# Optimization experiments

Hardware: AMD Instinct MI355X
Metric: run time of the kernel (lower is better)

The kernel has to match this reference:

```python
import jax, jax.numpy as jnp
import numpy as np

N, S, H = 16, 2048, 1024
K = 8           # num_models (experts)
D = H // 4      # bottleneck = hidden_dim // ds_factor


def setup_inputs() -> dict:
    key = jax.random.key(0)
    k1, k2, k3, k4, k5, k6 = jax.random.split(key, 6)
    hidden_states = jax.random.normal(k1, (N, S, H), dtype=jnp.float32)
    p = jax.random.uniform(k2, (N, K), dtype=jnp.float32)
    prob = p / jnp.sum(p, axis=-1, keepdims=True)  # normalized routing probs
    std = 0.02
    w_down = jax.random.normal(k3, (K, D, H), dtype=jnp.float32) * std
    b_down = jax.random.normal(k4, (K, D), dtype=jnp.float32) * std
    w_up = jax.random.normal(k5, (K, H, D), dtype=jnp.float32) * std
    b_up = jax.random.normal(k6, (K, H), dtype=jnp.float32) * std
    return {"hidden_states": hidden_states, "prob": prob,
            "w_down": w_down, "b_down": b_down,
            "w_up": w_up, "b_up": b_up}


def merge_linear(x, prob, weight, bias):
    # weight: (K, out, in); prob: (N, K) -> per-instance merged weight (N, out, in)
    w = jnp.einsum('nk,koi->noi', prob, weight)
    b = jnp.einsum('nk,ko->no', prob, bias)
    # x: (N, S, in) -> (N, S, out); matmul with per-instance weight^T
    y = jnp.einsum('nsi,noi->nso', x, w)
    return y + b[:, None, :]


def reference(hidden_states, prob, w_down, b_down, w_up, b_up):
    # MergeAdapter forward (ln_before=False, ln_after=False, dropout=0)
    residual = merge_linear(hidden_states, prob, w_down, b_down)
    residual = jax.nn.relu(residual)
    residual = merge_linear(residual, prob, w_up, b_up)
    return hidden_states + residual
```

## Files before the change

kernel.cpp:

```cpp
#include <hip/hip_runtime.h>


typedef unsigned short u16;
typedef __bf16 bf16x8 __attribute__((ext_vector_type(8)));
typedef float f32x4 __attribute__((ext_vector_type(4)));

__device__ __forceinline__ u16 f2bf(float f) {
    union { float f; unsigned int i; } v; v.f = f;
    unsigned int r = v.i + 0x7fffu + ((v.i >> 16) & 1u);
    return (u16)(r >> 16);
}

__device__ __forceinline__ void gload_lds16(const u16* g, u16* l) {
    __builtin_amdgcn_global_load_lds(
        (const __attribute__((address_space(1))) void*)g,
        (__attribute__((address_space(3))) void*)l,
        16, 0, 0);
}

__device__ __forceinline__ void store8(u16* dst, float4 a, float4 b) {
    union { uint4 u; u16 s[8]; } cv;
    cv.s[0]=f2bf(a.x); cv.s[1]=f2bf(a.y); cv.s[2]=f2bf(a.z); cv.s[3]=f2bf(a.w);
    cv.s[4]=f2bf(b.x); cv.s[5]=f2bf(b.y); cv.s[6]=f2bf(b.z); cv.s[7]=f2bf(b.w);
    *(uint4*)dst = cv.u;
}

__global__ __launch_bounds__(256)
void merge_kernel(const float* __restrict__ prob,
                  const float* __restrict__ w_down, const float* __restrict__ b_down,
                  const float* __restrict__ w_up,   const float* __restrict__ b_up,
                  u16* __restrict__ Wd, u16* __restrict__ Wu,
                  float* __restrict__ bd, float* __restrict__ bu)
{
    __shared__ float sp[128];
    const int tid = threadIdx.x;
    if (tid < 128) sp[tid] = prob[tid];
    __syncthreads();

    const int bid = blockIdx.x;
    const int E = 256 * 1024;

    if (bid < 256) {
        int v = bid * 256 + tid;
        const bool down = (v < 32768);
        const int vv = down ? v : (v - 32768);
        const float* W = down ? w_down : w_up;
        u16* O = down ? Wd : Wu;
        const size_t e = (size_t)vv * 8;

        float wf[8][8];
        #pragma unroll
        for (int k = 0; k < 8; ++k) {
            const float4 f0 = *(const float4*)(W + (size_t)k * E + e);
            const float4 f1 = *(const float4*)(W + (size_t)k * E + e + 4);
            wf[k][0] = f0.x; wf[k][1] = f0.y; wf[k][2] = f0.z; wf[k][3] = f0.w;
            wf[k][4] = f1.x; wf[k][5] = f1.y; wf[k][6] = f1.z; wf[k][7] = f1.w;
        }
        for (int n = 0; n < 16; ++n) {
            float a[8] = {0.f,0.f,0.f,0.f,0.f,0.f,0.f,0.f};
            #pragma unroll
            for (int k = 0; k < 8; ++k) {
                const float p = sp[n * 8 + k];
                #pragma unroll
                for (int j = 0; j < 8; ++j) a[j] = fmaf(p, wf[k][j], a[j]);
            }
            union { uint4 u; u16 s[8]; } ov;
            #pragma unroll
            for (int j = 0; j < 8; ++j) ov.s[j] = f2bf(a[j]);
            *(uint4*)(O + (size_t)n * E + e) = ov.u;
        }
    } else {
        int idx = (bid - 256) * 256 + tid;
        if (idx < 16 * 256) {
            const int n = idx >> 8, d = idx & 255;
            float s = 0.f;
            #pragma unroll
            for (int k = 0; k < 8; ++k)
                s = fmaf(sp[n * 8 + k], b_down[k * 256 + d], s);
            bd[idx] = s;
        } else {
            const int i2 = idx - 4096;
            const int n = i2 >> 10, h = i2 & 1023;
            float s = 0.f;
            #pragma unroll
            for (int k = 0; k < 8; ++k)
                s = fmaf(sp[n * 8 + k], b_up[k * 1024 + h], s);
            bu[i2] = s;
        }
    }
}

__global__ __launch_bounds__(512, 4)
void fused_adapter(const float* __restrict__ x, const u16* __restrict__ Wd,
                   const u16* __restrict__ Wu, const float* __restrict__ bd,
                   const float* __restrict__ bu, float* __restrict__ out)
{
    __shared__ __align__(16) u16 lds[40960];

    const int tid  = threadIdx.x;
    const int lane = tid & 63;
    const int wave = tid >> 6;
    const int quad = lane >> 4, rl = lane & 15;
    const int rxl  = rl & 7;

    const int id = blockIdx.x;
    const int batch = (id & 7) * 2 + ((id >> 3) & 1);
    const int mblk  = id >> 4;

    const float* xb  = x  + (size_t)batch * 2048 * 1024 + (size_t)mblk * 64 * 1024;
    const u16*   Wdb = Wd + (size_t)batch * 256 * 1024;
    const u16*   Wub = Wu + (size_t)batch * 1024 * 256;
    const float* bdb = bd + batch * 256;
    const float* bub = bu + batch * 1024;
    float*       ob  = out + (size_t)batch * 2048 * 1024 + (size_t)mblk * 64 * 1024;

    const int wm1 = wave >> 2, wn1 = wave & 3;

    u16* const b0x = lds;          u16* const b0w = lds + 4096;
    u16* const b1x = lds + 20480;  u16* const b1w = lds + 24576;

    const int xrow = tid >> 3, xsl = tid & 7;
    const int xdst = (xrow * 8 + (xsl ^ (xrow & 7))) * 8;
    const int wrow  = tid >> 3;
    const int wgcol = ((tid & 7) ^ (wrow & 7)) * 8;

    f32x4 acc1[2][4] = {};

    {
        const float4 a0 = *(const float4*)(xb + (size_t)xrow * 1024 + xsl * 8);
        const float4 a1 = *(const float4*)(xb + (size_t)xrow * 1024 + xsl * 8 + 4);
        #pragma unroll
        for (int r = 0; r < 4; ++r)
            gload_lds16(Wdb + (size_t)(r * 64 + wrow) * 1024 + wgcol,
                        b0w + (size_t)(r * 512 + wave * 64) * 8);
        store8(b0x + xdst, a0, a1);
    }
    __syncthreads();

    for (int it = 0; it < 16; ++it) {
        u16* cx = (it & 1) ? b1x : b0x;
        u16* cw = (it & 1) ? b1w : b0w;
        u16* nx = (it & 1) ? b0x : b1x;
        u16* nw = (it & 1) ? b0w : b1w;
        const int k1 = (it + 1) * 64;

        float4 a0, a1;
        if (it < 15) {
            a0 = *(const float4*)(xb + (size_t)xrow * 1024 + k1 + xsl * 8);
            a1 = *(const float4*)(xb + (size_t)xrow * 1024 + k1 + xsl * 8 + 4);
            #pragma unroll
            for (int r = 0; r < 4; ++r)
                gload_lds16(Wdb + (size_t)(r * 64 + wrow) * 1024 + k1 + wgcol,
                            nw + (size_t)(r * 512 + wave * 64) * 8);
        }

        #pragma unroll
        for (int kk = 0; kk < 64; kk += 32) {
            bf16x8 av[2], bv[4];
            #pragma unroll
            for (int mi = 0; mi < 2; ++mi)
                av[mi] = *(const bf16x8*)(cx + (wm1 * 32 + mi * 16 + rl) * 64
                                          + ((kk / 8 + quad) ^ rxl) * 8);
            #pragma unroll
            for (int ni = 0; ni < 4; ++ni)
                bv[ni] = *(const bf16x8*)(cw + (wn1 * 64 + ni * 16 + rl) * 64
                                          + ((kk / 8 + quad) ^ rxl) * 8);
            #pragma unroll
            for (int mi = 0; mi < 2; ++mi)
                #pragma unroll
                for (int ni = 0; ni < 4; ++ni)
                    acc1[mi][ni] = __builtin_amdgcn_mfma_f32_16x16x32_bf16(
                        av[mi], bv[ni], acc1[mi][ni], 0, 0, 0);
        }

        if (it < 15) store8(nx + xdst, a0, a1);
        __syncthreads();
    }

    #pragma unroll
    for (int ni = 0; ni < 4; ++ni) {
        const int col = wn1 * 64 + ni * 16 + rl;
        const float bval = bdb[col];
        const int lbc = col >> 3, hi = lbc & 24, c7 = lbc & 7, cl = col & 7;
        #pragma unroll
        for (int mi = 0; mi < 2; ++mi)
            #pragma unroll
            for (int i = 0; i < 4; ++i) {
                const int row = wm1 * 32 + mi * 16 + quad * 4 + i;
                const int phys = hi | (c7 ^ (row & 7));
                lds[row * 256 + phys * 8 + cl] =
                    f2bf(fmaxf(acc1[mi][ni][i] + bval, 0.0f));
            }
    }
    __syncthreads();

    const int wm2 = wave >> 2, wn2 = wave & 3;

    const int srow = tid >> 5, ss = tid & 31;
    const int wugcol = ((ss & 24) | ((ss & 7) ^ (srow & 7))) * 8;

    auto stage_wu = [&](int c, u16* buf) {
        #pragma unroll
        for (int rr = 0; rr < 4; ++rr)
            gload_lds16(Wub + (size_t)(c * 64 + rr * 16 + srow) * 256 + wugcol,
                        buf + (size_t)(rr * 512 + wave * 64) * 8);
    };

    stage_wu(0, lds + 16384);

    bf16x8 af[2][8];
    #pragma unroll
    for (int mi = 0; mi < 2; ++mi) {
        const int rowb = (wm2 * 32 + mi * 16 + rl) * 256;
        #pragma unroll
        for (int t = 0; t < 8; ++t) {
            const int lb = t * 4 + quad;
            const int phys = (lb & 24) | ((lb & 7) ^ rxl);
            af[mi][t] = *(const bf16x8*)(lds + rowb + phys * 8);
        }
    }
    __syncthreads();

    u16* cur = lds + 16384;
    u16* nxt = lds;
    for (int c = 0; c < 16; ++c) {
        if (c < 15) stage_wu(c + 1, nxt);

        f32x4 acc2[2] = {};
        #pragma unroll
        for (int t = 0; t < 8; ++t) {
            const int lb = t * 4 + quad;
            const int phys = (lb & 24) | ((lb & 7) ^ rxl);
            const bf16x8 bv = *(const bf16x8*)(cur + (wn2 * 16 + rl) * 256
                                               + phys * 8);
            #pragma unroll
            for (int mi = 0; mi < 2; ++mi)
                acc2[mi] = __builtin_amdgcn_mfma_f32_16x16x32_bf16(
                    af[mi][t], bv, acc2[mi], 0, 0, 0);
        }

        const int colg = c * 64 + wn2 * 16 + rl;
        const float bval = bub[colg];
        #pragma unroll
        for (int mi = 0; mi < 2; ++mi)
            #pragma unroll
            for (int i = 0; i < 4; ++i) {
                const int rowl = wm2 * 32 + mi * 16 + quad * 4 + i;
                const size_t off = (size_t)rowl * 1024 + colg;
                ob[off] = acc2[mi][i] + bval + xb[off];
            }

        if (c < 15) {
            u16* t2 = cur; cur = nxt; nxt = t2;
            __syncthreads();
        }
    }
}

extern "C" void kernel_launch(void* const* d_in, const int* in_sizes, int n_in,
                              void* d_out, int out_size, void* d_ws, size_t ws_size,
                              hipStream_t stream) {
    const float* hidden = (const float*)d_in[0];
    const float* prob   = (const float*)d_in[1];
    const float* w_down = (const float*)d_in[2];
    const float* b_down = (const float*)d_in[3];
    const float* w_up   = (const float*)d_in[4];
    const float* b_up   = (const float*)d_in[5];
    float* out = (float*)d_out;

    u16* Wd = (u16*)d_ws;
    u16* Wu = Wd + (size_t)16 * 256 * 1024;
    float* bd = (float*)(Wu + (size_t)16 * 1024 * 256);
    float* bu = bd + 16 * 256;

    merge_kernel<<<336, 256, 0, stream>>>(prob, w_down, b_down, w_up, b_up,
                                          Wd, Wu, bd, bu);

    fused_adapter<<<512, 512, 0, stream>>>(hidden, Wd, Wu, bd, bu, out);
}
```

Before: 320.4 us.

## Double M tile to 128 rows with triple-buffered K pipeline and manual waitcnts

Each block now processes 128 rows instead of 64, halving the grid and doubling per-block reuse of the merged down/up weights. The down-projection loop uses a three-stage LDS ring with explicit vmcnt/lgkmcnt waits and raw s_barrier in place of __syncthreads. The up-projection prefetches the residual x and bias into registers one chunk ahead. The aim is to cut weight reloads and barrier stalls, at the cost of more LDS (144KB), lower occupancy and fragile hand-counted wait values.

```diff
diff --git a/kernel.cpp b/kernel.cpp
--- a/kernel.cpp
+++ b/kernel.cpp
@@ -23,6 +23,14 @@
     cv.s[0]=f2bf(a.x); cv.s[1]=f2bf(a.y); cv.s[2]=f2bf(a.z); cv.s[3]=f2bf(a.w);
     cv.s[4]=f2bf(b.x); cv.s[5]=f2bf(b.y); cv.s[6]=f2bf(b.z); cv.s[7]=f2bf(b.w);
     *(uint4*)dst = cv.u;
+}
+
+#define MEMF() asm volatile("" ::: "memory")
+
+__device__ __forceinline__ void barx() {
+    asm volatile("" ::: "memory");
+    __builtin_amdgcn_s_barrier();
+    asm volatile("" ::: "memory");
 }
 
 __global__ __launch_bounds__(256)
@@ -90,12 +98,12 @@
     }
 }
 
-__global__ __launch_bounds__(512, 4)
+__global__ __launch_bounds__(512, 2)
 void fused_adapter(const float* __restrict__ x, const u16* __restrict__ Wd,
                    const u16* __restrict__ Wu, const float* __restrict__ bd,
                    const float* __restrict__ bu, float* __restrict__ out)
 {
-    __shared__ __align__(16) u16 lds[40960];
+    __shared__ __align__(16) u16 lds[73728];
 
     const int tid  = threadIdx.x;
     const int lane = tid & 63;
@@ -107,152 +115,205 @@
     const int batch = (id & 7) * 2 + ((id >> 3) & 1);
     const int mblk  = id >> 4;
 
-    const float* xb  = x  + (size_t)batch * 2048 * 1024 + (size_t)mblk * 64 * 1024;
+    const float* xb  = x  + (size_t)batch * 2048 * 1024 + (size_t)mblk * 128 * 1024;
     const u16*   Wdb = Wd + (size_t)batch * 256 * 1024;
     const u16*   Wub = Wu + (size_t)batch * 1024 * 256;
     const float* bdb = bd + batch * 256;
     const float* bub = bu + batch * 1024;
-    float*       ob  = out + (size_t)batch * 2048 * 1024 + (size_t)mblk * 64 * 1024;
+    float*       ob  = out + (size_t)batch * 2048 * 1024 + (size_t)mblk * 128 * 1024;
+
+    constexpr int XO[3] = {0, 24576, 49152};
+    constexpr int WO[3] = {8192, 32768, 57344};
 
     const int wm1 = wave >> 2, wn1 = wave & 3;
 
-    u16* const b0x = lds;          u16* const b0w = lds + 4096;
-    u16* const b1x = lds + 20480;  u16* const b1w = lds + 24576;
-
-    const int xrow = tid >> 3, xsl = tid & 7;
-    const int xdst = (xrow * 8 + (xsl ^ (xrow & 7))) * 8;
+    const int xrow = tid >> 2;
+    const int xcs  = (tid & 3) * 16;
+    const int s0   = (tid & 3) * 2;
+    const int xd0  = (xrow * 8 + (s0 ^ (xrow & 7))) * 8;
+    const int xd1  = (xrow * 8 + ((s0 + 1) ^ (xrow & 7))) * 8;
     const int wrow  = tid >> 3;
     const int wgcol = ((tid & 7) ^ (wrow & 7)) * 8;
 
-    f32x4 acc1[2][4] = {};
-
-    {
-        const float4 a0 = *(const float4*)(xb + (size_t)xrow * 1024 + xsl * 8);
-        const float4 a1 = *(const float4*)(xb + (size_t)xrow * 1024 + xsl * 8 + 4);
+    float bdv[4];
+    #pragma unroll
+    for (int ni = 0; ni < 4; ++ni) bdv[ni] = bdb[wn1 * 64 + ni * 16 + rl];
+    MEMF();
+
+    auto ldx = [&](int kt, float4* d) {
+        const float* p = xb + (size_t)xrow * 1024 + kt + xcs;
+        d[0] = *(const float4*)(p);
+        d[1] = *(const float4*)(p + 4);
+        d[2] = *(const float4*)(p + 8);
+        d[3] = *(const float4*)(p + 12);
+    };
+    auto stx = [&](u16* xbuf, const float4* d) {
+        store8(xbuf + xd0, d[0], d[1]);
+        store8(xbuf + xd1, d[2], d[3]);
+    };
+    auto stage_wd = [&](int kt, u16* wbuf) {
         #pragma unroll
         for (int r = 0; r < 4; ++r)
-            gload_lds16(Wdb + (size_t)(r * 64 + wrow) * 1024 + wgcol,
-                        b0w + (size_t)(r * 512 + wave * 64) * 8);
-        store8(b0x + xdst, a0, a1);
-    }
-    __syncthreads();
-
-    for (int it = 0; it < 16; ++it) {
-        u16* cx = (it & 1) ? b1x : b0x;
-        u16* cw = (it & 1) ? b1w : b0w;
-        u16* nx = (it & 1) ? b0x : b1x;
-        u16* nw = (it & 1) ? b0w : b1w;
-        const int k1 = (it + 1) * 64;
-
-        float4 a0, a1;
-        if (it < 15) {
-            a0 = *(const float4*)(xb + (size_t)xrow * 1024 + k1 + xsl * 8);
-            a1 = *(const float4*)(xb + (size_t)xrow * 1024 + k1 + xsl * 8 + 4);
-            #pragma unroll
-            for (int r = 0; r < 4; ++r)
-                gload_lds16(Wdb + (size_t)(r * 64 + wrow) * 1024 + k1 + wgcol,
-                            nw + (size_t)(r * 512 + wave * 64) * 8);
-        }
-
-        #pragma unroll
-        for (int kk = 0; kk < 64; kk += 32) {
-            bf16x8 av[2], bv[4];
-            #pragma unroll
-            for (int mi = 0; mi < 2; ++mi)
-                av[mi] = *(const bf16x8*)(cx + (wm1 * 32 + mi * 16 + rl) * 64
-                                          + ((kk / 8 + quad) ^ rxl) * 8);
-            #pragma unroll
-            for (int ni = 0; ni < 4; ++ni)
-                bv[ni] = *(const bf16x8*)(cw + (wn1 * 64 + ni * 16 + rl) * 64
-                                          + ((kk / 8 + quad) ^ rxl) * 8);
-            #pragma unroll
-            for (int mi = 0; mi < 2; ++mi)
+            gload_lds16(Wdb + (size_t)(r * 64 + wrow) * 1024 + kt + wgcol,
+                        wbuf + r * 4096 + wave * 512);
+    };
+
+    f32x4 acc1[4][4] = {};
+    auto comp1 = [&](const u16* xbuf, const u16* wbuf) {
+        #pragma unroll
+        for (int kk = 0; kk < 2; ++kk) {
+            bf16x8 av[4], bv[4];
+            #pragma unroll
+            for (int mi = 0; mi < 4; ++mi) {
+                const int row = wm1 * 64 + mi * 16 + rl;
+                av[mi] = *(const bf16x8*)(xbuf + (row * 8 + ((kk * 4 + quad) ^ rxl)) * 8);
+            }
+            #pragma unroll
+            for (int ni = 0; ni < 4; ++ni) {
+                const int row = wn1 * 64 + ni * 16 + rl;
+                bv[ni] = *(const bf16x8*)(wbuf + (row * 8 + ((kk * 4 + quad) ^ rxl)) * 8);
+            }
+            #pragma unroll
+            for (int mi = 0; mi < 4; ++mi)
                 #pragma unroll
                 for (int ni = 0; ni < 4; ++ni)
                     acc1[mi][ni] = __builtin_amdgcn_mfma_f32_16x16x32_bf16(
                         av[mi], bv[ni], acc1[mi][ni], 0, 0, 0);
         }
-
-        if (it < 15) store8(nx + xdst, a0, a1);
-        __syncthreads();
-    }
+    };
+
+    float4 xa[2][4];
+    ldx(0, xa[0]);  stage_wd(0, lds + WO[0]);
+    MEMF();
+    ldx(64, xa[1]); stage_wd(64, lds + WO[1]);
+    asm volatile("s_waitcnt vmcnt(12)" ::: "memory");
+    stx(lds + XO[0], xa[0]);
+    asm volatile("s_waitcnt vmcnt(8)" ::: "memory");
+    asm volatile("s_waitcnt lgkmcnt(0)" ::: "memory");
+    barx();
+
+    #pragma unroll
+    for (int t = 0; t < 16; ++t) {
+        const int cb = t % 3, nb1 = (t + 1) % 3, nb2 = (t + 2) % 3;
+        if (t < 14) {
+            ldx((t + 2) * 64, xa[t & 1]);
+            stage_wd((t + 2) * 64, lds + WO[nb2]);
+        }
+        comp1(lds + XO[cb], lds + WO[cb]);
+        if (t < 14)       asm volatile("s_waitcnt vmcnt(8)" ::: "memory");
+        else if (t == 14) asm volatile("s_waitcnt vmcnt(0)" ::: "memory");
+        if (t < 15) {
+            stx(lds + XO[nb1], xa[(t + 1) & 1]);
+            asm volatile("s_waitcnt lgkmcnt(0)" ::: "memory");
+        }
+        barx();
+    }
+
+    const int wm2 = wave >> 1, wn2 = wave & 1;
+    const int srow = tid >> 5, ss = tid & 31;
+    const int wugcol = ((ss & 24) | ((ss & 7) ^ (srow & 7))) * 8;
+    u16* const wub0 = lds + 32768;
+    u16* const wub1 = lds + 49152;
+
+    auto stage_wu = [&](int c, u16* buf) {
+        #pragma unroll
+        for (int rr = 0; rr < 4; ++rr)
+            gload_lds16(Wub + (size_t)(c * 64 + rr * 16 + srow) * 256 + wugcol,
+                        buf + rr * 4096 + wave * 512);
+    };
+    auto ldxqb = [&](int c, float* dq) {
+        #pragma unroll
+        for (int ni = 0; ni < 2; ++ni) {
+            const int colg = c * 64 + wn2 * 32 + ni * 16 + rl;
+            #pragma unroll
+            for (int mi = 0; mi < 2; ++mi)
+                #pragma unroll
+                for (int i = 0; i < 4; ++i)
+                    dq[ni * 8 + mi * 4 + i] =
+                        xb[(size_t)(wm2 * 32 + mi * 16 + quad * 4 + i) * 1024 + colg];
+            dq[16 + ni] = bub[colg];
+        }
+    };
+
+    stage_wu(0, wub0);
+    MEMF();
+    float xqb[2][18];
+    ldxqb(0, xqb[0]);
 
     #pragma unroll
     for (int ni = 0; ni < 4; ++ni) {
         const int col = wn1 * 64 + ni * 16 + rl;
-        const float bval = bdb[col];
         const int lbc = col >> 3, hi = lbc & 24, c7 = lbc & 7, cl = col & 7;
         #pragma unroll
-        for (int mi = 0; mi < 2; ++mi)
+        for (int mi = 0; mi < 4; ++mi)
             #pragma unroll
             for (int i = 0; i < 4; ++i) {
-                const int row = wm1 * 32 + mi * 16 + quad * 4 + i;
+                const int row = wm1 * 64 + mi * 16 + quad * 4 + i;
                 const int phys = hi | (c7 ^ (row & 7));
                 lds[row * 256 + phys * 8 + cl] =
-                    f2bf(fmaxf(acc1[mi][ni][i] + bval, 0.0f));
-            }
-    }
-    __syncthreads();
-
-    const int wm2 = wave >> 2, wn2 = wave & 3;
-
-    const int srow = tid >> 5, ss = tid & 31;
-    const int wugcol = ((ss & 24) | ((ss & 7) ^ (srow & 7))) * 8;
-
-    auto stage_wu = [&](int c, u16* buf) {
-        #pragma unroll
-        for (int rr = 0; rr < 4; ++rr)
-            gload_lds16(Wub + (size_t)(c * 64 + rr * 16 + srow) * 256 + wugcol,
-                        buf + (size_t)(rr * 512 + wave * 64) * 8);
-    };
-
-    stage_wu(0, lds + 16384);
+                    f2bf(fmaxf(acc1[mi][ni][i] + bdv[ni], 0.0f));
+            }
+    }
+    asm volatile("s_waitcnt lgkmcnt(0)" ::: "memory");
+    asm volatile("s_waitcnt vmcnt(18)" ::: "memory");
+    barx();
 
     bf16x8 af[2][8];
     #pragma unroll
     for (int mi = 0; mi < 2; ++mi) {
-        const int rowb = (wm2 * 32 + mi * 16 + rl) * 256;
+        const int row = wm2 * 32 + mi * 16 + rl;
         #pragma unroll
         for (int t = 0; t < 8; ++t) {
             const int lb = t * 4 + quad;
             const int phys = (lb & 24) | ((lb & 7) ^ rxl);
-            af[mi][t] = *(const bf16x8*)(lds + rowb + phys * 8);
-        }
-    }
-    __syncthreads();
-
-    u16* cur = lds + 16384;
-    u16* nxt = lds;
+            af[mi][t] = *(const bf16x8*)(lds + (row * 32 + phys) * 8);
+        }
+    }
+
+    #pragma unroll
     for (int c = 0; c < 16; ++c) {
-        if (c < 15) stage_wu(c + 1, nxt);
-
-        f32x4 acc2[2] = {};
+        const u16* wcur = (c & 1) ? wub1 : wub0;
+        if (c < 15) {
+            ldxqb(c + 1, xqb[(c + 1) & 1]);
+            MEMF();
+            stage_wu(c + 1, (c & 1) ? wub0 : wub1);
+        }
+        f32x4 acc2[2][2] = {};
         #pragma unroll
         for (int t = 0; t < 8; ++t) {
-            const int lb = t * 4 + quad;
-            const int phys = (lb & 24) | ((lb & 7) ^ rxl);
-            const bf16x8 bv = *(const bf16x8*)(cur + (wn2 * 16 + rl) * 256
-                                               + phys * 8);
+            bf16x8 bv[2];
+            #pragma unroll
+            for (int ni = 0; ni < 2; ++ni) {
+                const int row = wn2 * 32 + ni * 16 + rl;
+                const int lb = t * 4 + quad;
+                const int phys = (lb & 24) | ((lb & 7) ^ rxl);
+                bv[ni] = *(const bf16x8*)(wcur + (row * 32 + phys) * 8);
+            }
             #pragma unroll
             for (int mi = 0; mi < 2; ++mi)
-                acc2[mi] = __builtin_amdgcn_mfma_f32_16x16x32_bf16(
-                    af[mi][t], bv, acc2[mi], 0, 0, 0);
-        }
-
-        const int colg = c * 64 + wn2 * 16 + rl;
-        const float bval = bub[colg];
-        #pragma unroll
-        for (int mi = 0; mi < 2; ++mi)
-            #pragma unroll
-            for (int i = 0; i < 4; ++i) {
-                const int rowl = wm2 * 32 + mi * 16 + quad * 4 + i;
-                const size_t off = (size_t)rowl * 1024 + colg;
-                ob[off] = acc2[mi][i] + bval + xb[off];
-            }
-
+                #pragma unroll
+                for (int ni = 0; ni < 2; ++ni)
+                    acc2[mi][ni] = __builtin_amdgcn_mfma_f32_16x16x32_bf16(
+                        af[mi][t], bv[ni], acc2[mi][ni], 0, 0, 0);
+        }
+        if (c < 15) asm volatile("s_waitcnt vmcnt(22)" ::: "memory");
+
+        #pragma unroll
+        for (int ni = 0; ni < 2; ++ni) {
+            const int colg = c * 64 + wn2 * 32 + ni * 16 + rl;
+            const float bval = xqb[c & 1][16 + ni];
+            #pragma unroll
+            for (int mi = 0; mi < 2; ++mi)
+                #pragma unroll
+                for (int i = 0; i < 4; ++i) {
+                    const int rowl = wm2 * 32 + mi * 16 + quad * 4 + i;
+                    ob[(size_t)rowl * 1024 + colg] =
+                        acc2[mi][ni][i] + bval + xqb[c & 1][ni * 8 + mi * 4 + i];
+                }
+        }
         if (c < 15) {
-            u16* t2 = cur; cur = nxt; nxt = t2;
-            __syncthreads();
+            asm volatile("s_waitcnt vmcnt(16)" ::: "memory");
+            barx();
         }
     }
 }
@@ -276,5 +337,5 @@
     merge_kernel<<<336, 256, 0, stream>>>(prob, w_down, b_down, w_up, b_up,
                                           Wd, Wu, bd, bu);
 
-    fused_adapter<<<512, 512, 0, stream>>>(hidden, Wd, Wu, bd, bu, out);
-}
+    fused_adapter<<<256, 512, 0, stream>>>(hidden, Wd, Wu, bd, bu, out);
+}
```

Result: faster. 300.3 us (-6.3%).

## Triple-buffer down-proj K loop with manual waitcnt and prefetch residual loads

Applied to the files above, without the earlier changes.

Restructures the first GEMM loop to use K-steps of 32 with a three-stage LDS ring buffer and prefetch distance two. Full __syncthreads are replaced with raw s_barrier plus hand-placed vmcnt/lgkmcnt waits, and s_setprio is raised around the MFMA blocks. In the up-projection loop the residual x and bias values are prefetched one chunk ahead into registers, and the down bias is hoisted. LDS usage shrinks, which may allow more blocks per CU, but the hand-counted wait counts are fragile and a miscount would cause races.

```diff
diff --git a/kernel.cpp b/kernel.cpp
--- a/kernel.cpp
+++ b/kernel.cpp
@@ -18,11 +18,18 @@
         16, 0, 0);
 }
 
-__device__ __forceinline__ void store8(u16* dst, float4 a, float4 b) {
-    union { uint4 u; u16 s[8]; } cv;
+__device__ __forceinline__ void store4(u16* dst, float4 a) {
+    union { uint2 u; u16 s[4]; } cv;
     cv.s[0]=f2bf(a.x); cv.s[1]=f2bf(a.y); cv.s[2]=f2bf(a.z); cv.s[3]=f2bf(a.w);
-    cv.s[4]=f2bf(b.x); cv.s[5]=f2bf(b.y); cv.s[6]=f2bf(b.z); cv.s[7]=f2bf(b.w);
-    *(uint4*)dst = cv.u;
+    *(uint2*)dst = cv.u;
+}
+
+#define MEMF() asm volatile("" ::: "memory")
+
+__device__ __forceinline__ void barx() {
+    asm volatile("" ::: "memory");
+    __builtin_amdgcn_s_barrier();
+    asm volatile("" ::: "memory");
 }
 
 __global__ __launch_bounds__(256)
@@ -95,7 +102,7 @@
                    const u16* __restrict__ Wu, const float* __restrict__ bd,
                    const float* __restrict__ bu, float* __restrict__ out)
 {
-    __shared__ __align__(16) u16 lds[40960];
+    __shared__ __align__(16) u16 lds[32768];
 
     const int tid  = threadIdx.x;
     const int lane = tid & 63;
@@ -114,73 +121,117 @@
     const float* bub = bu + batch * 1024;
     float*       ob  = out + (size_t)batch * 2048 * 1024 + (size_t)mblk * 64 * 1024;
 
+    constexpr int XO[3] = {0, 10240, 20480};
+    constexpr int WO[3] = {2048, 12288, 22528};
+
     const int wm1 = wave >> 2, wn1 = wave & 3;
 
-    u16* const b0x = lds;          u16* const b0w = lds + 4096;
-    u16* const b1x = lds + 20480;  u16* const b1w = lds + 24576;
-
-    const int xrow = tid >> 3, xsl = tid & 7;
-    const int xdst = (xrow * 8 + (xsl ^ (xrow & 7))) * 8;
-    const int wrow  = tid >> 3;
-    const int wgcol = ((tid & 7) ^ (wrow & 7)) * 8;
+    const int xrow = tid >> 3;
+    const int xc4  = (tid & 7) * 4;
+    const int xs2  = (tid & 7) >> 1, xhalf = tid & 1;
+    const int xdst = xrow * 32 + (xs2 ^ (xrow & 3)) * 8 + xhalf * 4;
+    const int wswz = ((lane & 3) ^ ((lane >> 2) & 3)) * 8;
+
+    float bdv[4];
+    #pragma unroll
+    for (int ni = 0; ni < 4; ++ni) bdv[ni] = bdb[wn1 * 64 + ni * 16 + rl];
+    asm volatile("s_waitcnt vmcnt(0)" ::: "memory");
+
+    auto ldx = [&](int kt, float4& d) {
+        d = *(const float4*)(xb + (size_t)xrow * 1024 + kt + xc4);
+    };
+    auto stx = [&](u16* xbuf, const float4& d) { store4(xbuf + xdst, d); };
+    auto stage_wd = [&](int kt, u16* wbuf) {
+        #pragma unroll
+        for (int r = 0; r < 2; ++r)
+            gload_lds16(Wdb + (size_t)((wave * 2 + r) * 16 + (lane >> 2)) * 1024
+                            + kt + wswz,
+                        wbuf + (wave * 2 + r) * 512);
+    };
 
     f32x4 acc1[2][4] = {};
-
-    {
-        const float4 a0 = *(const float4*)(xb + (size_t)xrow * 1024 + xsl * 8);
-        const float4 a1 = *(const float4*)(xb + (size_t)xrow * 1024 + xsl * 8 + 4);
-        #pragma unroll
-        for (int r = 0; r < 4; ++r)
-            gload_lds16(Wdb + (size_t)(r * 64 + wrow) * 1024 + wgcol,
-                        b0w + (size_t)(r * 512 + wave * 64) * 8);
-        store8(b0x + xdst, a0, a1);
-    }
-    __syncthreads();
-
-    for (int it = 0; it < 16; ++it) {
-        u16* cx = (it & 1) ? b1x : b0x;
-        u16* cw = (it & 1) ? b1w : b0w;
-        u16* nx = (it & 1) ? b0x : b1x;
-        u16* nw = (it & 1) ? b0w : b1w;
-        const int k1 = (it + 1) * 64;
-
-        float4 a0, a1;
-        if (it < 15) {
-            a0 = *(const float4*)(xb + (size_t)xrow * 1024 + k1 + xsl * 8);
-            a1 = *(const float4*)(xb + (size_t)xrow * 1024 + k1 + xsl * 8 + 4);
-            #pragma unroll
-            for (int r = 0; r < 4; ++r)
-                gload_lds16(Wdb + (size_t)(r * 64 + wrow) * 1024 + k1 + wgcol,
-                            nw + (size_t)(r * 512 + wave * 64) * 8);
-        }
-
-        #pragma unroll
-        for (int kk = 0; kk < 64; kk += 32) {
-            bf16x8 av[2], bv[4];
-            #pragma unroll
-            for (int mi = 0; mi < 2; ++mi)
-                av[mi] = *(const bf16x8*)(cx + (wm1 * 32 + mi * 16 + rl) * 64
-                                          + ((kk / 8 + quad) ^ rxl) * 8);
+    auto comp1 = [&](const u16* xbuf, const u16* wbuf) {
+        bf16x8 av[2], bv[4];
+        #pragma unroll
+        for (int mi = 0; mi < 2; ++mi) {
+            const int row = wm1 * 32 + mi * 16 + rl;
+            av[mi] = *(const bf16x8*)(xbuf + row * 32 + (quad ^ (row & 3)) * 8);
+        }
+        #pragma unroll
+        for (int ni = 0; ni < 4; ++ni) {
+            const int row = wn1 * 64 + ni * 16 + rl;
+            bv[ni] = *(const bf16x8*)(wbuf + row * 32 + (quad ^ (row & 3)) * 8);
+        }
+        __builtin_amdgcn_s_setprio(1);
+        #pragma unroll
+        for (int mi = 0; mi < 2; ++mi)
             #pragma unroll
             for (int ni = 0; ni < 4; ++ni)
-                bv[ni] = *(const bf16x8*)(cw + (wn1 * 64 + ni * 16 + rl) * 64
-                                          + ((kk / 8 + quad) ^ rxl) * 8);
-            #pragma unroll
-            for (int mi = 0; mi < 2; ++mi)
-                #pragma unroll
-                for (int ni = 0; ni < 4; ++ni)
-                    acc1[mi][ni] = __builtin_amdgcn_mfma_f32_16x16x32_bf16(
-                        av[mi], bv[ni], acc1[mi][ni], 0, 0, 0);
-        }
-
-        if (it < 15) store8(nx + xdst, a0, a1);
-        __syncthreads();
-    }
+                acc1[mi][ni] = __builtin_amdgcn_mfma_f32_16x16x32_bf16(
+                    av[mi], bv[ni], acc1[mi][ni], 0, 0, 0);
+        __builtin_amdgcn_s_setprio(0);
+    };
+
+    float4 xa[2];
+    ldx(0, xa[0]);  stage_wd(0, lds + WO[0]);
+    MEMF();
+    ldx(32, xa[1]); stage_wd(32, lds + WO[1]);
+    asm volatile("s_waitcnt vmcnt(5)" ::: "memory");
+    stx(lds + XO[0], xa[0]);
+    asm volatile("s_waitcnt vmcnt(3)" ::: "memory");
+    asm volatile("s_waitcnt lgkmcnt(0)" ::: "memory");
+    barx();
+
+    #pragma unroll
+    for (int t = 0; t < 32; ++t) {
+        const int cb = t % 3;
+        if (t < 30) {
+            ldx((t + 2) * 32, xa[t & 1]);
+            stage_wd((t + 2) * 32, lds + WO[(t + 2) % 3]);
+            MEMF();
+        }
+        comp1(lds + XO[cb], lds + WO[cb]);
+        if (t < 30)       asm volatile("s_waitcnt vmcnt(3)" ::: "memory");
+        else if (t == 30) asm volatile("s_waitcnt vmcnt(0)" ::: "memory");
+        if (t < 31) {
+            stx(lds + XO[(t + 1) % 3], xa[(t + 1) & 1]);
+            asm volatile("s_waitcnt lgkmcnt(0)" ::: "memory");
+        }
+        barx();
+    }
+
+    const int wm2 = wave >> 2, wn2 = wave & 3;
+    const int srow = tid >> 5, ss = tid & 31;
+    const int wugcol = ((ss & 24) | ((ss & 7) ^ (srow & 7))) * 8;
+    u16* const wub0 = lds + 16384;
+    u16* const wub1 = lds;
+
+    auto stage_wu = [&](int c, u16* buf) {
+        #pragma unroll
+        for (int rr = 0; rr < 4; ++rr)
+            gload_lds16(Wub + (size_t)(c * 64 + rr * 16 + srow) * 256 + wugcol,
+                        buf + (size_t)(rr * 512 + wave * 64) * 8);
+    };
+    auto ldxqb = [&](int c, float* dq) {
+        const int colg = c * 64 + wn2 * 16 + rl;
+        #pragma unroll
+        for (int mi = 0; mi < 2; ++mi)
+            #pragma unroll
+            for (int i = 0; i < 4; ++i)
+                dq[mi * 4 + i] =
+                    xb[(size_t)(wm2 * 32 + mi * 16 + quad * 4 + i) * 1024 + colg];
+        dq[8] = bub[colg];
+    };
+
+    stage_wu(0, wub0);
+    MEMF();
+    float xq[2][9];
+    ldxqb(0, xq[0]);
+    MEMF();
 
     #pragma unroll
     for (int ni = 0; ni < 4; ++ni) {
         const int col = wn1 * 64 + ni * 16 + rl;
-        const float bval = bdb[col];
         const int lbc = col >> 3, hi = lbc & 24, c7 = lbc & 7, cl = col & 7;
         #pragma unroll
         for (int mi = 0; mi < 2; ++mi)
@@ -189,70 +240,67 @@
                 const int row = wm1 * 32 + mi * 16 + quad * 4 + i;
                 const int phys = hi | (c7 ^ (row & 7));
                 lds[row * 256 + phys * 8 + cl] =
-                    f2bf(fmaxf(acc1[mi][ni][i] + bval, 0.0f));
+                    f2bf(fmaxf(acc1[mi][ni][i] + bdv[ni], 0.0f));
             }
     }
-    __syncthreads();
-
-    const int wm2 = wave >> 2, wn2 = wave & 3;
-
-    const int srow = tid >> 5, ss = tid & 31;
-    const int wugcol = ((ss & 24) | ((ss & 7) ^ (srow & 7))) * 8;
-
-    auto stage_wu = [&](int c, u16* buf) {
-        #pragma unroll
-        for (int rr = 0; rr < 4; ++rr)
-            gload_lds16(Wub + (size_t)(c * 64 + rr * 16 + srow) * 256 + wugcol,
-                        buf + (size_t)(rr * 512 + wave * 64) * 8);
-    };
-
-    stage_wu(0, lds + 16384);
+    asm volatile("s_waitcnt lgkmcnt(0)" ::: "memory");
+    asm volatile("s_waitcnt vmcnt(9)" ::: "memory");
+    barx();
 
     bf16x8 af[2][8];
     #pragma unroll
     for (int mi = 0; mi < 2; ++mi) {
-        const int rowb = (wm2 * 32 + mi * 16 + rl) * 256;
+        const int row = wm2 * 32 + mi * 16 + rl;
         #pragma unroll
         for (int t = 0; t < 8; ++t) {
             const int lb = t * 4 + quad;
             const int phys = (lb & 24) | ((lb & 7) ^ rxl);
-            af[mi][t] = *(const bf16x8*)(lds + rowb + phys * 8);
-        }
-    }
-    __syncthreads();
-
-    u16* cur = lds + 16384;
-    u16* nxt = lds;
+            af[mi][t] = *(const bf16x8*)(lds + (row * 32 + phys) * 8);
+        }
+    }
+    asm volatile("s_waitcnt lgkmcnt(0)" ::: "memory");
+    barx();
+
+    #pragma unroll
     for (int c = 0; c < 16; ++c) {
-        if (c < 15) stage_wu(c + 1, nxt);
-
+        const u16* wcur = (c & 1) ? wub1 : wub0;
+        if (c < 15) {
+            ldxqb(c + 1, xq[(c + 1) & 1]);
+            MEMF();
+            stage_wu(c + 1, (c & 1) ? wub0 : wub1);
+            MEMF();
+        }
         f32x4 acc2[2] = {};
+        __builtin_amdgcn_s_setprio(1);
         #pragma unroll
         for (int t = 0; t < 8; ++t) {
             const int lb = t * 4 + quad;
             const int phys = (lb & 24) | ((lb & 7) ^ rxl);
-            const bf16x8 bv = *(const bf16x8*)(cur + (wn2 * 16 + rl) * 256
+            const bf16x8 bv = *(const bf16x8*)(wcur + (wn2 * 16 + rl) * 256
                                                + phys * 8);
             #pragma unroll
             for (int mi = 0; mi < 2; ++mi)
                 acc2[mi] = __builtin_amdgcn_mfma_f32_16x16x32_bf16(
                     af[mi][t], bv, acc2[mi], 0, 0, 0);
         }
-
-        const int colg = c * 64 + wn2 * 16 + rl;
-        const float bval = bub[colg];
-        #pragma unroll
-        for (int mi = 0; mi < 2; ++mi)
-            #pragma unroll
-            for (int i = 0; i < 4; ++i) {
-                const int rowl = wm2 * 32 + mi * 16 + quad * 4 + i;
-                const size_t off = (size_t)rowl * 1024 + colg;
-                ob[off] = acc2[mi][i] + bval + xb[off];
-            }
-
+        __builtin_amdgcn_s_setprio(0);
+        if (c == 0) asm volatile("s_waitcnt vmcnt(13)" ::: "memory");
+
+        {
+            const int colg = c * 64 + wn2 * 16 + rl;
+            const float bval = xq[c & 1][8];
+            #pragma unroll
+            for (int mi = 0; mi < 2; ++mi)
+                #pragma unroll
+                for (int i = 0; i < 4; ++i) {
+                    const int rowl = wm2 * 32 + mi * 16 + quad * 4 + i;
+                    ob[(size_t)rowl * 1024 + colg] =
+                        acc2[mi][i] + bval + xq[c & 1][mi * 4 + i];
+                }
+        }
         if (c < 15) {
-            u16* t2 = cur; cur = nxt; nxt = t2;
-            __syncthreads();
+            asm volatile("s_waitcnt vmcnt(8)" ::: "memory");
+            barx();
         }
     }
 }
```

Measured after the change: 463.2 us. 44.6% more time.

## Split fused adapter into separate down and up projection kernels with bf16 intermediate

Applied to the files above, without the earlier changes.

Replaces the single fused down+up kernel with a down kernel that writes the ReLU bottleneck activations to a bf16 workspace, and an up kernel over many more blocks that tiles the output columns. The down kernel now loads x straight from global into registers and converts it to bf16 there, instead of staging it through LDS. The aim is more parallelism and occupancy in the up projection, which had a long serial loop per block. The cost is an extra pass reading x for the residual, plus the intermediate write and read.

```diff
diff --git a/kernel.cpp b/kernel.cpp
--- a/kernel.cpp
+++ b/kernel.cpp
@@ -9,6 +9,13 @@
     union { float f; unsigned int i; } v; v.f = f;
     unsigned int r = v.i + 0x7fffu + ((v.i >> 16) & 1u);
     return (u16)(r >> 16);
+}
+
+__device__ __forceinline__ bf16x8 cvt8(float4 a, float4 b) {
+    union { bf16x8 v; u16 s[8]; } r;
+    r.s[0]=f2bf(a.x); r.s[1]=f2bf(a.y); r.s[2]=f2bf(a.z); r.s[3]=f2bf(a.w);
+    r.s[4]=f2bf(b.x); r.s[5]=f2bf(b.y); r.s[6]=f2bf(b.z); r.s[7]=f2bf(b.w);
+    return r.v;
 }
 
 __device__ __forceinline__ void gload_lds16(const u16* g, u16* l) {
@@ -16,13 +23,6 @@
         (const __attribute__((address_space(1))) void*)g,
         (__attribute__((address_space(3))) void*)l,
         16, 0, 0);
-}
-
-__device__ __forceinline__ void store8(u16* dst, float4 a, float4 b) {
-    union { uint4 u; u16 s[8]; } cv;
-    cv.s[0]=f2bf(a.x); cv.s[1]=f2bf(a.y); cv.s[2]=f2bf(a.z); cv.s[3]=f2bf(a.w);
-    cv.s[4]=f2bf(b.x); cv.s[5]=f2bf(b.y); cv.s[6]=f2bf(b.z); cv.s[7]=f2bf(b.w);
-    *(uint4*)dst = cv.u;
 }
 
 __global__ __launch_bounds__(256)
@@ -90,18 +90,16 @@
     }
 }
 
-__global__ __launch_bounds__(512, 4)
-void fused_adapter(const float* __restrict__ x, const u16* __restrict__ Wd,
-                   const u16* __restrict__ Wu, const float* __restrict__ bd,
-                   const float* __restrict__ bu, float* __restrict__ out)
+__global__ __launch_bounds__(256, 2)
+void down_kernel(const float* __restrict__ x, const u16* __restrict__ Wd,
+                 const float* __restrict__ bd, u16* __restrict__ R)
 {
-    __shared__ __align__(16) u16 lds[40960];
+    __shared__ __align__(16) u16 wdl[2][8192];
 
     const int tid  = threadIdx.x;
     const int lane = tid & 63;
     const int wave = tid >> 6;
     const int quad = lane >> 4, rl = lane & 15;
-    const int rxl  = rl & 7;
 
     const int id = blockIdx.x;
     const int batch = (id & 7) * 2 + ((id >> 3) & 1);
@@ -109,151 +107,158 @@
 
     const float* xb  = x  + (size_t)batch * 2048 * 1024 + (size_t)mblk * 64 * 1024;
     const u16*   Wdb = Wd + (size_t)batch * 256 * 1024;
-    const u16*   Wub = Wu + (size_t)batch * 1024 * 256;
     const float* bdb = bd + batch * 256;
-    const float* bub = bu + batch * 1024;
-    float*       ob  = out + (size_t)batch * 2048 * 1024 + (size_t)mblk * 64 * 1024;
-
-    const int wm1 = wave >> 2, wn1 = wave & 3;
-
-    u16* const b0x = lds;          u16* const b0w = lds + 4096;
-    u16* const b1x = lds + 20480;  u16* const b1w = lds + 24576;
-
-    const int xrow = tid >> 3, xsl = tid & 7;
-    const int xdst = (xrow * 8 + (xsl ^ (xrow & 7))) * 8;
-    const int wrow  = tid >> 3;
-    const int wgcol = ((tid & 7) ^ (wrow & 7)) * 8;
-
-    f32x4 acc1[2][4] = {};
-
-    {
-        const float4 a0 = *(const float4*)(xb + (size_t)xrow * 1024 + xsl * 8);
-        const float4 a1 = *(const float4*)(xb + (size_t)xrow * 1024 + xsl * 8 + 4);
-        #pragma unroll
-        for (int r = 0; r < 4; ++r)
-            gload_lds16(Wdb + (size_t)(r * 64 + wrow) * 1024 + wgcol,
-                        b0w + (size_t)(r * 512 + wave * 64) * 8);
-        store8(b0x + xdst, a0, a1);
-    }
+    u16*         Rb  = R  + (size_t)batch * 2048 * 256 + (size_t)mblk * 64 * 256;
+
+    float bdv[4];
+    #pragma unroll
+    for (int ni = 0; ni < 4; ++ni) bdv[ni] = bdb[wave * 64 + ni * 16 + rl];
+
+    const int srow = lane >> 2, sslot = lane & 3;
+    auto stage = [&](int it, int b) {
+        const int kt = it * 32;
+        #pragma unroll
+        for (int r = 0; r < 4; ++r) {
+            const int row = r * 64 + wave * 16 + srow;
+            gload_lds16(Wdb + (size_t)row * 1024 + kt + ((sslot ^ (row & 3)) * 8),
+                        wdl[b] + r * 2048 + wave * 512);
+        }
+    };
+
+    auto ldA = [&](int it, bf16x8* av) {
+        #pragma unroll
+        for (int mi = 0; mi < 4; ++mi) {
+            const float* p = xb + (size_t)(mi * 16 + rl) * 1024 + it * 32 + quad * 8;
+            av[mi] = cvt8(*(const float4*)p, *(const float4*)(p + 4));
+        }
+    };
+
+    f32x4 acc[4][4] = {};
+    auto comp = [&](const u16* buf, const bf16x8* av) {
+        #pragma unroll
+        for (int ni = 0; ni < 4; ++ni) {
+            const int c = wave * 64 + ni * 16 + rl;
+            const bf16x8 bv = *(const bf16x8*)(buf + c * 32 + (quad ^ (rl & 3)) * 8);
+            #pragma unroll
+            for (int mi = 0; mi < 4; ++mi)
+                acc[mi][ni] = __builtin_amdgcn_mfma_f32_16x16x32_bf16(
+                    av[mi], bv, acc[mi][ni], 0, 0, 0);
+        }
+    };
+
+    bf16x8 avA[4], avB[4];
+    ldA(0, avA);
+    stage(0, 0);
     __syncthreads();
 
-    for (int it = 0; it < 16; ++it) {
-        u16* cx = (it & 1) ? b1x : b0x;
-        u16* cw = (it & 1) ? b1w : b0w;
-        u16* nx = (it & 1) ? b0x : b1x;
-        u16* nw = (it & 1) ? b0w : b1w;
-        const int k1 = (it + 1) * 64;
-
-        float4 a0, a1;
-        if (it < 15) {
-            a0 = *(const float4*)(xb + (size_t)xrow * 1024 + k1 + xsl * 8);
-            a1 = *(const float4*)(xb + (size_t)xrow * 1024 + k1 + xsl * 8 + 4);
-            #pragma unroll
-            for (int r = 0; r < 4; ++r)
-                gload_lds16(Wdb + (size_t)(r * 64 + wrow) * 1024 + k1 + wgcol,
-                            nw + (size_t)(r * 512 + wave * 64) * 8);
-        }
-
-        #pragma unroll
-        for (int kk = 0; kk < 64; kk += 32) {
-            bf16x8 av[2], bv[4];
-            #pragma unroll
-            for (int mi = 0; mi < 2; ++mi)
-                av[mi] = *(const bf16x8*)(cx + (wm1 * 32 + mi * 16 + rl) * 64
-                                          + ((kk / 8 + quad) ^ rxl) * 8);
-            #pragma unroll
-            for (int ni = 0; ni < 4; ++ni)
-                bv[ni] = *(const bf16x8*)(cw + (wn1 * 64 + ni * 16 + rl) * 64
-                                          + ((kk / 8 + quad) ^ rxl) * 8);
-            #pragma unroll
-            for (int mi = 0; mi < 2; ++mi)
+    #pragma unroll 2
+    for (int p = 0; p < 16; ++p) {
+        const int e = 2 * p;
+        if (e < 31) { stage(e + 1, 1); ldA(e + 1, avB); }
+        comp(wdl[0], avA);
+        __syncthreads();
+        const int o = e + 1;
+        if (o < 31) { stage(o + 1, 0); ldA(o + 1, avA); }
+        comp(wdl[1], avB);
+        __syncthreads();
+    }
+
+    #pragma unroll
+    for (int ni = 0; ni < 4; ++ni) {
+        const int col = wave * 64 + ni * 16 + rl;
+        #pragma unroll
+        for (int mi = 0; mi < 4; ++mi)
+            #pragma unroll
+            for (int i = 0; i < 4; ++i) {
+                const int row = mi * 16 + quad * 4 + i;
+                Rb[(size_t)row * 256 + col] =
+                    f2bf(fmaxf(acc[mi][ni][i] + bdv[ni], 0.0f));
+            }
+    }
+}
+
+__global__ __launch_bounds__(256, 4)
+void up_kernel(const float* __restrict__ x, const u16* __restrict__ Wu,
+               const float* __restrict__ bu, const u16* __restrict__ R,
+               float* __restrict__ out)
+{
+    __shared__ __align__(16) u16 wul[2][8192];
+
+    const int tid  = threadIdx.x;
+    const int lane = tid & 63;
+    const int wave = tid >> 6;
+    const int quad = lane >> 4, rl = lane & 15;
+
+    const int id = blockIdx.x;
+    const int batch = (id & 7) * 2 + ((id >> 3) & 1);
+    const int rest  = id >> 4;
+    const int mblk  = rest & 31;
+    const int nblk  = rest >> 5;
+
+    const u16* Rb = R + (size_t)batch * 2048 * 256 + (size_t)mblk * 64 * 256;
+    const size_t base = (size_t)batch * 2048 * 1024 + (size_t)mblk * 64 * 1024
+                      + (size_t)nblk * 128;
+    const float* xb  = x + base;
+    float*       ob  = out + base;
+    const u16*   Wub = Wu + (size_t)batch * 1024 * 256 + (size_t)nblk * 128 * 256;
+    const float* bub2 = bu + batch * 1024 + nblk * 128;
+
+    float buv[2];
+    #pragma unroll
+    for (int ni = 0; ni < 2; ++ni) buv[ni] = bub2[wave * 32 + ni * 16 + rl];
+
+    const int srow = lane >> 3, sslot = lane & 7;
+    auto stage = [&](int it, int b) {
+        const int kt = it * 64;
+        #pragma unroll
+        for (int r = 0; r < 4; ++r) {
+            const int row = r * 32 + wave * 8 + srow;
+            gload_lds16(Wub + (size_t)row * 256 + kt + ((sslot ^ (row & 7)) * 8),
+                        wul[b] + r * 2048 + wave * 512);
+        }
+    };
+
+    f32x4 acc[4][2] = {};
+
+    stage(0, 0);
+    __syncthreads();
+
+    #pragma unroll
+    for (int it = 0; it < 4; ++it) {
+        const int cur = it & 1;
+        if (it < 3) stage(it + 1, cur ^ 1);
+        #pragma unroll
+        for (int kk = 0; kk < 2; ++kk) {
+            bf16x8 av[4];
+            #pragma unroll
+            for (int mi = 0; mi < 4; ++mi)
+                av[mi] = *(const bf16x8*)(Rb + (size_t)(mi * 16 + rl) * 256
+                                          + it * 64 + kk * 32 + quad * 8);
+            #pragma unroll
+            for (int ni = 0; ni < 2; ++ni) {
+                const int c = wave * 32 + ni * 16 + rl;
+                const bf16x8 bv = *(const bf16x8*)(wul[cur] + c * 64
+                                    + (((kk * 4 + quad) ^ (rl & 7)) * 8));
                 #pragma unroll
-                for (int ni = 0; ni < 4; ++ni)
-                    acc1[mi][ni] = __builtin_amdgcn_mfma_f32_16x16x32_bf16(
-                        av[mi], bv[ni], acc1[mi][ni], 0, 0, 0);
-        }
-
-        if (it < 15) store8(nx + xdst, a0, a1);
+                for (int mi = 0; mi < 4; ++mi)
+                    acc[mi][ni] = __builtin_amdgcn_mfma_f32_16x16x32_bf16(
+                        av[mi], bv, acc[mi][ni], 0, 0, 0);
+            }
+        }
         __syncthreads();
     }
 
     #pragma unroll
-    for (int ni = 0; ni < 4; ++ni) {
-        const int col = wn1 * 64 + ni * 16 + rl;
-        const float bval = bdb[col];
-        const int lbc = col >> 3, hi = lbc & 24, c7 = lbc & 7, cl = col & 7;
-        #pragma unroll
-        for (int mi = 0; mi < 2; ++mi)
+    for (int ni = 0; ni < 2; ++ni) {
+        const int coll = wave * 32 + ni * 16 + rl;
+        #pragma unroll
+        for (int mi = 0; mi < 4; ++mi)
             #pragma unroll
             for (int i = 0; i < 4; ++i) {
-                const int row = wm1 * 32 + mi * 16 + quad * 4 + i;
-                const int phys = hi | (c7 ^ (row & 7));
-                lds[row * 256 + phys * 8 + cl] =
-                    f2bf(fmaxf(acc1[mi][ni][i] + bval, 0.0f));
-            }
-    }
-    __syncthreads();
-
-    const int wm2 = wave >> 2, wn2 = wave & 3;
-
-    const int srow = tid >> 5, ss = tid & 31;
-    const int wugcol = ((ss & 24) | ((ss & 7) ^ (srow & 7))) * 8;
-
-    auto stage_wu = [&](int c, u16* buf) {
-        #pragma unroll
-        for (int rr = 0; rr < 4; ++rr)
-            gload_lds16(Wub + (size_t)(c * 64 + rr * 16 + srow) * 256 + wugcol,
-                        buf + (size_t)(rr * 512 + wave * 64) * 8);
-    };
-
-    stage_wu(0, lds + 16384);
-
-    bf16x8 af[2][8];
-    #pragma unroll
-    for (int mi = 0; mi < 2; ++mi) {
-        const int rowb = (wm2 * 32 + mi * 16 + rl) * 256;
-        #pragma unroll
-        for (int t = 0; t < 8; ++t) {
-            const int lb = t * 4 + quad;
-            const int phys = (lb & 24) | ((lb & 7) ^ rxl);
-            af[mi][t] = *(const bf16x8*)(lds + rowb + phys * 8);
-        }
-    }
-    __syncthreads();
-
-    u16* cur = lds + 16384;
-    u16* nxt = lds;
-    for (int c = 0; c < 16; ++c) {
-        if (c < 15) stage_wu(c + 1, nxt);
-
-        f32x4 acc2[2] = {};
-        #pragma unroll
-        for (int t = 0; t < 8; ++t) {
-            const int lb = t * 4 + quad;
-            const int phys = (lb & 24) | ((lb & 7) ^ rxl);
-            const bf16x8 bv = *(const bf16x8*)(cur + (wn2 * 16 + rl) * 256
-                                               + phys * 8);
-            #pragma unroll
-            for (int mi = 0; mi < 2; ++mi)
-                acc2[mi] = __builtin_amdgcn_mfma_f32_16x16x32_bf16(
-                    af[mi][t], bv, acc2[mi], 0, 0, 0);
-        }
-
-        const int colg = c * 64 + wn2 * 16 + rl;
-        const float bval = bub[colg];
-        #pragma unroll
-        for (int mi = 0; mi < 2; ++mi)
-            #pragma unroll
-            for (int i = 0; i < 4; ++i) {
-                const int rowl = wm2 * 32 + mi * 16 + quad * 4 + i;
-                const size_t off = (size_t)rowl * 1024 + colg;
-                ob[off] = acc2[mi][i] + bval + xb[off];
-            }
-
-        if (c < 15) {
-            u16* t2 = cur; cur = nxt; nxt = t2;
-            __syncthreads();
-        }
+                const int rowl = mi * 16 + quad * 4 + i;
+                const size_t off = (size_t)rowl * 1024 + coll;
+                ob[off] = acc[mi][ni][i] + buv[ni] + xb[off];
+            }
     }
 }
 
@@ -272,9 +277,12 @@
     u16* Wu = Wd + (size_t)16 * 256 * 1024;
     float* bd = (float*)(Wu + (size_t)16 * 1024 * 256);
     float* bu = bd + 16 * 256;
+    u16* R  = (u16*)(bu + 16 * 1024);
 
     merge_kernel<<<336, 256, 0, stream>>>(prob, w_down, b_down, w_up, b_up,
                                           Wd, Wu, bd, bu);
 
-    fused_adapter<<<512, 512, 0, stream>>>(hidden, Wd, Wu, bd, bu, out);
-}
+    down_kernel<<<512, 256, 0, stream>>>(hidden, Wd, bd, R);
+
+    up_kernel<<<4096, 256, 0, stream>>>(hidden, Wu, bu, R, out);
+}
```

Measured after the change: 396.9 us. 1.24x slower.
